# Optimization experiments

Measured on AMD Instinct MI355X. Metric: run time of the kernel, lower is better.

The kernel has to match this reference:

```python
import jax, jax.numpy as jnp
import numpy as np
import math

B, LC, LQ, D = 64, 1024, 128, 128


def setup_inputs() -> dict:
    key = jax.random.key(0)
    k1, k2, k3, k4, k5 = jax.random.split(key, 5)
    c_rep = jax.random.normal(k1, (B, LC, D), dtype=jnp.float32)
    q_rep = jax.random.normal(k2, (B, LQ, D), dtype=jnp.float32)
    c_mask = jax.random.randint(k3, (B, LC), 0, 2, dtype=jnp.int32)
    q_mask = jax.random.randint(k4, (B, LQ), 0, 2, dtype=jnp.int32)
    lim = math.sqrt(1.0 / D)
    w = jax.random.uniform(k5, (3 * D,), dtype=jnp.float32, minval=-lim, maxval=lim)
    return {"c_rep": c_rep, "q_rep": q_rep, "c_mask": c_mask, "q_mask": q_mask, "w": w}


def _mask_logits(t, m):
    # mask == 1 means masked (matches original: target*(1-mask) + mask*-1e30)
    return t * (1.0 - m) + m * (-1e30)


def reference(c_rep, q_rep, c_mask, q_mask, w):
    d = c_rep.shape[-1]
    w1, w2, w3 = w[:d], w[d:2 * d], w[2 * d:]
    # Trilinear similarity S[b,i,j] = <ct,w1> + <qt,w2> + <ct*qt,w3>
    # computed without materializing the [B,Lc,Lq,3D] concat tensor.
    S = (c_rep @ w1)[:, :, None] \
        + (q_rep @ w2)[:, None, :] \
        + jnp.einsum('bid,bjd->bij', c_rep * w3, q_rep)  # [B, Lc, Lq]
    qm = q_mask[:, None, :].astype(S.dtype)  # [B, 1, Lq]
    cm = c_mask[:, :, None].astype(S.dtype)  # [B, Lc, 1]
    S1 = jax.nn.softmax(_mask_logits(S, qm), axis=2)  # softmax over query dim
    S2 = jax.nn.softmax(_mask_logits(S, cm), axis=1)  # softmax over context dim
    A = jnp.einsum('bij,bjd->bid', S1, q_rep)  # [B, Lc, D]
    # B_att = S1 @ S2^T @ c_rep, associated right-first to avoid [B,Lc,Lc]
    T = jnp.einsum('bkj,bkd->bjd', S2, c_rep)  # [B, Lq, D]
    B_att = jnp.einsum('bij,bjd->bid', S1, T)  # [B, Lc, D]
    out = jnp.concatenate([c_rep, A, c_rep * A, c_rep * B_att], axis=2)  # [B, Lc, 4D]
    # dropout is identity at inference
    return out
```

## Files before the change

kernel.cpp:

```cpp
#include <hip/hip_runtime.h>
#include <hip/hip_bf16.h>
#include <cstdint>
#include <cstddef>

#define B_   64
#define LC_  1024
#define LQ_  128
#define D_   128

typedef __bf16 bf16;
typedef bf16  bf16x8 __attribute__((ext_vector_type(8)));
typedef bf16  bf16x4 __attribute__((ext_vector_type(4)));
typedef float f32x4  __attribute__((ext_vector_type(4)));

__device__ __forceinline__ f32x4 mfma16(bf16x8 a, bf16x8 b, f32x4 c) {
  return __builtin_amdgcn_mfma_f32_16x16x32_bf16(a, b, c, 0, 0, 0);
}

__device__ __forceinline__ int swz(int row, int elem) { return elem ^ ((row & 7) << 3); }

__global__ __launch_bounds__(256) void kpre(const float* __restrict__ c, const float* __restrict__ q,
                                            const float* __restrict__ w,
                                            float* __restrict__ cw1, bf16* __restrict__ cw3,
                                            bf16* __restrict__ cT,
                                            float* __restrict__ qw2, bf16* __restrict__ qb,
                                            bf16* __restrict__ qT) {
  __shared__ float wA[128];
  __shared__ float wB[128];
  __shared__ bf16  tile[128 * 136];
  const int b = blockIdx.y, bx = blockIdx.x;
  const int t = threadIdx.x;

  if (bx < 8) {
    const int k0 = bx * 128;
    if (t < 128) { wA[t] = w[t]; wB[t] = w[256 + t]; }
    __syncthreads();
    {
      const int r = t >> 1, d0 = (t & 1) * 64;
      const float* crow = c + ((size_t)(b * LC_ + k0 + r) * D_ + d0);
      bf16* orow = cw3 + ((size_t)(b * LC_ + k0 + r) * D_ + d0);
      float dot = 0.f;
#pragma unroll
      for (int v = 0; v < 8; ++v) {
        const float4 f0 = ((const float4*)crow)[v * 2 + 0];
        const float4 f1 = ((const float4*)crow)[v * 2 + 1];
        const int dd = d0 + v * 8;
        dot += f0.x * wA[dd + 0] + f0.y * wA[dd + 1] + f0.z * wA[dd + 2] + f0.w * wA[dd + 3]
             + f1.x * wA[dd + 4] + f1.y * wA[dd + 5] + f1.z * wA[dd + 6] + f1.w * wA[dd + 7];
        bf16x8 oc, o;
        oc[0] = (bf16)f0.x; oc[1] = (bf16)f0.y; oc[2] = (bf16)f0.z; oc[3] = (bf16)f0.w;
        oc[4] = (bf16)f1.x; oc[5] = (bf16)f1.y; oc[6] = (bf16)f1.z; oc[7] = (bf16)f1.w;
        o[0] = (bf16)(f0.x * wB[dd + 0]); o[1] = (bf16)(f0.y * wB[dd + 1]);
        o[2] = (bf16)(f0.z * wB[dd + 2]); o[3] = (bf16)(f0.w * wB[dd + 3]);
        o[4] = (bf16)(f1.x * wB[dd + 4]); o[5] = (bf16)(f1.y * wB[dd + 5]);
        o[6] = (bf16)(f1.z * wB[dd + 6]); o[7] = (bf16)(f1.w * wB[dd + 7]);
        *(bf16x8*)&tile[r * 136 + dd] = oc;
        *(bf16x8*)(orow + v * 8) = o;
      }
      dot += __shfl_xor(dot, 1);
      if ((t & 1) == 0) cw1[b * LC_ + k0 + r] = dot;
    }
    __syncthreads();
    {
      const int d = t >> 1, kh = (t & 1) * 64;
      bf16* trow = cT + ((size_t)(b * D_ + d) * LC_ + k0 + kh);
#pragma unroll
      for (int v = 0; v < 8; ++v) {
        bf16x8 o;
#pragma unroll
        for (int e = 0; e < 8; ++e) o[e] = tile[(kh + v * 8 + e) * 136 + d];
        *(bf16x8*)(trow + v * 8) = o;
      }
    }
  } else {
    if (t < 128) wA[t] = w[128 + t];
    __syncthreads();
    {
      const int r = t >> 1, d0 = (t & 1) * 64;
      const float* qrow = q + ((size_t)(b * LQ_ + r) * D_ + d0);
      bf16* orow = qb + ((size_t)(b * LQ_ + r) * D_ + d0);
      float dot = 0.f;
#pragma unroll
      for (int v = 0; v < 8; ++v) {
        const float4 f0 = ((const float4*)qrow)[v * 2 + 0];
        const float4 f1 = ((const float4*)qrow)[v * 2 + 1];
        const int dd = d0 + v * 8;
        dot += f0.x * wA[dd + 0] + f0.y * wA[dd + 1] + f0.z * wA[dd + 2] + f0.w * wA[dd + 3]
             + f1.x * wA[dd + 4] + f1.y * wA[dd + 5] + f1.z * wA[dd + 6] + f1.w * wA[dd + 7];
        bf16x8 o;
        o[0] = (bf16)f0.x; o[1] = (bf16)f0.y; o[2] = (bf16)f0.z; o[3] = (bf16)f0.w;
        o[4] = (bf16)f1.x; o[5] = (bf16)f1.y; o[6] = (bf16)f1.z; o[7] = (bf16)f1.w;
        *(bf16x8*)&tile[r * 136 + dd] = o;
        *(bf16x8*)(orow + v * 8) = o;
      }
      dot += __shfl_xor(dot, 1);
      if ((t & 1) == 0) qw2[b * LQ_ + r] = dot;
    }
    __syncthreads();
    {
      const int d = t >> 1, jh = (t & 1) * 64;
      bf16* trow = qT + ((size_t)(b * D_ + d) * LQ_ + jh);
#pragma unroll
      for (int v = 0; v < 8; ++v) {
        bf16x8 o;
#pragma unroll
        for (int e = 0; e < 8; ++e) o[e] = tile[(jh + v * 8 + e) * 136 + d];
        *(bf16x8*)(trow + v * 8) = o;
      }
    }
  }
}

__global__ __launch_bounds__(256) void k1(const float* __restrict__ cw1, const float* __restrict__ qw2,
                                          const int* __restrict__ cmask,
                                          const bf16* __restrict__ cw3, const bf16* __restrict__ cT,
                                          const bf16* __restrict__ qb,
                                          float* __restrict__ Tpart, float* __restrict__ lpart) {
  __shared__ bf16  qs[64 * 128];
  __shared__ bf16  PT[64 * 64];
  __shared__ float lred[4][64];
  const int bx = blockIdx.x;
  const int ks = bx >> 1, jh = bx & 1;
  const int b = blockIdx.y;
  const int j0g = jh * 64;
  const int t = threadIdx.x;
  const int wk = t >> 6, lane = t & 63, quad = lane >> 4, l15 = lane & 15;

#pragma unroll
  for (int idx = t; idx < 1024; idx += 256) {
    const int row = idx >> 4, ch = idx & 15;
    *(bf16x8*)&qs[row * 128 + swz(row, ch * 8)] =
        *(const bf16x8*)(qb + ((size_t)(b * LQ_ + j0g + row) * D_ + ch * 8));
  }
  const f32x4 z = {0.f, 0.f, 0.f, 0.f};
  f32x4 Tacc[4][2];
#pragma unroll
  for (int jt = 0; jt < 4; ++jt) { Tacc[jt][0] = z; Tacc[jt][1] = z; }
  float lacc[4] = {0.f, 0.f, 0.f, 0.f};
  float qv[4];
#pragma unroll
  for (int jt = 0; jt < 4; ++jt) qv[jt] = qw2[b * LQ_ + j0g + jt * 16 + l15];
  __syncthreads();

  for (int kt = 0; kt < 2; ++kt) {
    const int k0g = ks * 128 + kt * 64;

    f32x4 S[4] = {z, z, z, z};
#pragma unroll
    for (int kk = 0; kk < 4; ++kk) {
      const bf16x8 a = *(const bf16x8*)(cw3 +
          ((size_t)(b * LC_ + k0g + wk * 16 + l15) * D_ + kk * 32 + quad * 8));
#pragma unroll
      for (int jt = 0; jt < 4; ++jt) {
        const int jr = jt * 16 + l15;
        const bf16x8 bq = *(const bf16x8*)&qs[jr * 128 + swz(jr, kk * 32 + quad * 8)];
        S[jt] = mfma16(a, bq, S[jt]);
      }
    }
    float c1v[4]; int cmv[4];
#pragma unroll
    for (int rr = 0; rr < 4; ++rr) {
      const int krow = k0g + wk * 16 + quad * 4 + rr;
      c1v[rr] = cw1[b * LC_ + krow];
      cmv[rr] = cmask[b * LC_ + krow];
    }
#pragma unroll
    for (int jt = 0; jt < 4; ++jt) {
      bf16x4 pk;
#pragma unroll
      for (int rr = 0; rr < 4; ++rr) {
        const float p = cmv[rr] ? 0.f : __expf(S[jt][rr] + c1v[rr] + qv[jt]);
        lacc[jt] += p;
        pk[rr] = (bf16)p;
      }
      const int jr = jt * 16 + l15;
      *(bf16x4*)&PT[jr * 64 + swz(jr, wk * 16 + quad * 4)] = pk;
    }
    __syncthreads();

#pragma unroll
    for (int kk = 0; kk < 2; ++kk) {
      const bf16x8 bd0 = *(const bf16x8*)(cT +
          ((size_t)(b * D_ + wk * 32 + l15) * LC_ + k0g + kk * 32 + quad * 8));
      const bf16x8 bd1 = *(const bf16x8*)(cT +
          ((size_t)(b * D_ + wk * 32 + 16 + l15) * LC_ + k0g + kk * 32 + quad * 8));
#pragma unroll
      for (int jt = 0; jt < 4; ++jt) {
        const int jr = jt * 16 + l15;
        const bf16x8 aP = *(const bf16x8*)&PT[jr * 64 + swz(jr, kk * 32 + quad * 8)];
        Tacc[jt][0] = mfma16(aP, bd0, Tacc[jt][0]);
        Tacc[jt][1] = mfma16(aP, bd1, Tacc[jt][1]);
      }
    }
    __syncthreads();
  }

#pragma unroll
  for (int jt = 0; jt < 4; ++jt) {
    lacc[jt] += __shfl_xor(lacc[jt], 16);
    lacc[jt] += __shfl_xor(lacc[jt], 32);
  }
  if (lane < 16) {
#pragma unroll
    for (int jt = 0; jt < 4; ++jt) lred[wk][jt * 16 + l15] = lacc[jt];
  }
  __syncthreads();
  if (t < 64)
    lpart[(size_t)(b * 8 + ks) * 128 + j0g + t] =
        lred[0][t] + lred[1][t] + lred[2][t] + lred[3][t];

  float* tp = Tpart + ((size_t)(b * 8 + ks)) * (128 * 128);
#pragma unroll
  for (int jt = 0; jt < 4; ++jt)
#pragma unroll
    for (int dt = 0; dt < 2; ++dt)
#pragma unroll
      for (int rr = 0; rr < 4; ++rr)
        tp[(j0g + jt * 16 + quad * 4 + rr) * 128 + wk * 32 + dt * 16 + l15] =
            Tacc[jt][dt][rr];
}

__global__ __launch_bounds__(512) void k1r(const float* __restrict__ Tpart,
                                           const float* __restrict__ lpart,
                                           bf16* __restrict__ TT) {
  __shared__ float Tsum[32 * 132];
  __shared__ float linv[32];
  const int js = blockIdx.x, b = blockIdx.y;
  const int j0 = js * 32;
  const int t = threadIdx.x;
#pragma unroll
  for (int idx = t; idx < 1024; idx += 512) {
    const int row = idx >> 5, seg = idx & 31;
    float4 s = {0.f, 0.f, 0.f, 0.f};
#pragma unroll
    for (int i = 0; i < 8; ++i) {
      const float4 v = ((const float4*)(Tpart + ((size_t)(b * 8 + i)) * (128 * 128)) + j0 * 32)[idx];
      s.x += v.x; s.y += v.y; s.z += v.z; s.w += v.w;
    }
    *(float4*)&Tsum[row * 132 + seg * 4] = s;
  }
  if (t < 32) {
    float l = 0.f;
#pragma unroll
    for (int i = 0; i < 8; ++i) l += lpart[(size_t)(b * 8 + i) * 128 + j0 + t];
    linv[t] = 1.f / l;
  }
  __syncthreads();
  if (t < 256) {
    const int d = t >> 1, jhh = (t & 1) * 16;
    bf16x8 o0, o1;
#pragma unroll
    for (int e = 0; e < 8; ++e) {
      o0[e] = (bf16)(Tsum[(jhh + e) * 132 + d] * linv[jhh + e]);
      o1[e] = (bf16)(Tsum[(jhh + 8 + e) * 132 + d] * linv[jhh + 8 + e]);
    }
    bf16* dst = TT + ((size_t)(b * D_ + d) * LQ_ + j0 + jhh);
    *(bf16x8*)dst = o0;
    *(bf16x8*)(dst + 8) = o1;
  }
}

__global__ __launch_bounds__(256, 4) void k2(const float* __restrict__ c, const float* __restrict__ cw1,
                                             const float* __restrict__ qw2, const int* __restrict__ qmask,
                                             const bf16* __restrict__ cw3, const bf16* __restrict__ qb,
                                             const bf16* __restrict__ qT, const bf16* __restrict__ TT,
                                             float* __restrict__ out) {
  __shared__ __align__(16) char smem[37888];
  bf16* qTs = (bf16*)(smem);
  bf16* TTs = (bf16*)(smem + 16384);
  bf16* P1  = (bf16*)(smem + 32768);
  float* A32 = (float*)(smem);
  float* B32 = (float*)(smem + 16896);
  const int it = blockIdx.x, b = blockIdx.y;
  const int i0 = it * 64;
  const int t = threadIdx.x;
  const int w = t >> 6, lane = t & 63, quad = lane >> 4, l15 = lane & 15;

  bf16x8 aF[4];
#pragma unroll
  for (int kk = 0; kk < 4; ++kk)
    aF[kk] = *(const bf16x8*)(cw3 +
        ((size_t)(b * LC_ + i0 + w * 16 + l15) * D_ + kk * 32 + quad * 8));
  float c1v[4];
#pragma unroll
  for (int rr = 0; rr < 4; ++rr)
    c1v[rr] = cw1[b * LC_ + i0 + w * 16 + quad * 4 + rr];

  const f32x4 z = {0.f, 0.f, 0.f, 0.f};
  f32x4 Aacc[8], Bacc[8];
#pragma unroll
  for (int n = 0; n < 8; ++n) { Aacc[n] = z; Bacc[n] = z; }
  float lacc[4] = {0.f, 0.f, 0.f, 0.f};

#pragma unroll
  for (int jh = 0; jh < 2; ++jh) {
#pragma unroll
    for (int idx = t; idx < 1024; idx += 256) {
      const int row = idx >> 3, ch = idx & 7;
      const int sc = (ch * 8) ^ ((row & 7) << 3);
      *(bf16x8*)&qTs[row * 64 + sc] =
          *(const bf16x8*)(qT + ((size_t)(b * D_ + row) * LQ_ + jh * 64 + ch * 8));
      *(bf16x8*)&TTs[row * 64 + sc] =
          *(const bf16x8*)(TT + ((size_t)(b * D_ + row) * LQ_ + jh * 64 + ch * 8));
    }
    __syncthreads();

#pragma unroll
    for (int jtl = 0; jtl < 2; ++jtl) {
      const int j0 = jh * 64 + jtl * 32;
      const float qv0 = qw2[b * LQ_ + j0 + l15];
      const float qv1 = qw2[b * LQ_ + j0 + 16 + l15];
      const int   qm0 = qmask[b * LQ_ + j0 + l15];
      const int   qm1 = qmask[b * LQ_ + j0 + 16 + l15];

      f32x4 S0 = z, S1 = z;
#pragma unroll
      for (int kk = 0; kk < 4; ++kk) {
        const bf16x8 b0 = *(const bf16x8*)(qb +
            ((size_t)(b * LQ_ + j0 + l15) * D_ + kk * 32 + quad * 8));
        const bf16x8 b1 = *(const bf16x8*)(qb +
            ((size_t)(b * LQ_ + j0 + 16 + l15) * D_ + kk * 32 + quad * 8));
        S0 = mfma16(aF[kk], b0, S0);
        S1 = mfma16(aF[kk], b1, S1);
      }
#pragma unroll
      for (int rr = 0; rr < 4; ++rr) {
        const float p0 = qm0 ? 0.f : __expf(S0[rr] + c1v[rr] + qv0);
        const float p1 = qm1 ? 0.f : __expf(S1[rr] + c1v[rr] + qv1);
        lacc[rr] += p0 + p1;
        P1[(w * 16 + quad * 4 + rr) * 40 + l15] = (bf16)p0;
        P1[(w * 16 + quad * 4 + rr) * 40 + 16 + l15] = (bf16)p1;
      }
      __syncthreads();

      const bf16x8 aP = *(bf16x8*)&P1[(w * 16 + l15) * 40 + quad * 8];
      const int cbase = jtl * 32 + quad * 8;
#pragma unroll
      for (int nt = 0; nt < 8; ++nt) {
        const int row = nt * 16 + l15;
        const int sc = cbase ^ ((row & 7) << 3);
        const bf16x8 bq = *(bf16x8*)&qTs[row * 64 + sc];
        const bf16x8 bt = *(bf16x8*)&TTs[row * 64 + sc];
        Aacc[nt] = mfma16(aP, bq, Aacc[nt]);
        Bacc[nt] = mfma16(aP, bt, Bacc[nt]);
      }
      __syncthreads();
    }
  }

#pragma unroll
  for (int rr = 0; rr < 4; ++rr) {
    float v = lacc[rr];
    v += __shfl_xor(v, 1); v += __shfl_xor(v, 2);
    v += __shfl_xor(v, 4); v += __shfl_xor(v, 8);
    lacc[rr] = 1.f / v;
  }

#pragma unroll
  for (int h = 0; h < 2; ++h) {
    if ((w >> 1) == h) {
      const int lrow0 = (w & 1) * 16 + quad * 4;
#pragma unroll
      for (int nt = 0; nt < 8; ++nt)
#pragma unroll
        for (int rr = 0; rr < 4; ++rr) {
          A32[(lrow0 + rr) * 132 + nt * 16 + l15] = Aacc[nt][rr] * lacc[rr];
          B32[(lrow0 + rr) * 132 + nt * 16 + l15] = Bacc[nt][rr] * lacc[rr];
        }
    }
    __syncthreads();
#pragma unroll
    for (int idx = t; idx < 1024; idx += 256) {
      const int lrow = idx >> 5, seg = idx & 31;
      const size_t grow = (size_t)(b * LC_ + i0 + h * 32 + lrow);
      const float4 c4 = ((const float4*)(c + grow * D_))[seg];
      const float4 a4 = *(float4*)&A32[lrow * 132 + seg * 4];
      const float4 b4 = *(float4*)&B32[lrow * 132 + seg * 4];
      float4* ob = (float4*)(out + grow * 512);
      ob[seg] = c4;
      ob[32 + seg] = a4;
      float4 ca; ca.x = c4.x * a4.x; ca.y = c4.y * a4.y; ca.z = c4.z * a4.z; ca.w = c4.w * a4.w;
      ob[64 + seg] = ca;
      float4 cb; cb.x = c4.x * b4.x; cb.y = c4.y * b4.y; cb.z = c4.z * b4.z; cb.w = c4.w * b4.w;
      ob[96 + seg] = cb;
    }
    __syncthreads();
  }
}

extern "C" void kernel_launch(void* const* d_in, const int* in_sizes, int n_in,
                              void* d_out, int out_size, void* d_ws, size_t ws_size,
                              hipStream_t stream) {
  (void)in_sizes; (void)n_in; (void)out_size; (void)ws_size;
  const float* c     = (const float*)d_in[0];
  const float* q     = (const float*)d_in[1];
  const int*   cmask = (const int*)d_in[2];
  const int*   qmask = (const int*)d_in[3];
  const float* w     = (const float*)d_in[4];
  float* out = (float*)d_out;

  char* ws = (char*)d_ws;
  float* cw1 = (float*)(ws + 0);
  float* qw2 = (float*)(ws + 262144);
  bf16*  cw3 = (bf16*)(ws + 294912);
  bf16*  cT  = (bf16*)(ws + 17072128);
  bf16*  qb  = (bf16*)(ws + 33849344);
  bf16*  qT  = (bf16*)(ws + 35946496);
  bf16*  TT  = (bf16*)(ws + 38043648);

  float* Tpart = out;
  float* lpart = out + 8388608;

  kpre<<<dim3(9, 64), 256, 0, stream>>>(c, q, w, cw1, cw3, cT, qw2, qb, qT);
  k1  <<<dim3(16, 64), 256, 0, stream>>>(cw1, qw2, cmask, cw3, cT, qb, Tpart, lpart);
  k1r <<<dim3(4, 64), 512, 0, stream>>>(Tpart, lpart, TT);
  k2  <<<dim3(16, 64), 256, 0, stream>>>(c, cw1, qw2, qmask, cw3, qb, qT, TT, out);
}
```

Measured before the change: 237.7 us.

## Drop transposed context copy; feed T-GEMM directly from fp32 context via K16 MFMA

The preprocessing kernel no longer writes a bf16 transposed copy of the context. k1 now builds the T = S2^T·C product straight from register-held P fragments and strided fp32 context loads, converted on the fly for a 16x16x16 MFMA. This removes the shared-memory P round-trip and its barriers. k1's grid is re-split into 32 query-row slices per batch, with the per-warp T partials reduced through shared-memory atomics. Separately, k2 drops two barriers per inner step. The price is uncoalesced strided global loads of c, shared atomics and more blocks, and the k2 barrier removal risks a race on the P1 buffer.

```diff
diff --git a/kernel.cpp b/kernel.cpp
--- a/kernel.cpp
+++ b/kernel.cpp
@@ -12,9 +12,22 @@
 typedef bf16  bf16x8 __attribute__((ext_vector_type(8)));
 typedef bf16  bf16x4 __attribute__((ext_vector_type(4)));
 typedef float f32x4  __attribute__((ext_vector_type(4)));
+typedef short s16x4  __attribute__((ext_vector_type(4)));
 
 __device__ __forceinline__ f32x4 mfma16(bf16x8 a, bf16x8 b, f32x4 c) {
   return __builtin_amdgcn_mfma_f32_16x16x32_bf16(a, b, c, 0, 0, 0);
+}
+__device__ __forceinline__ f32x4 mfma16k16(s16x4 a, s16x4 b, f32x4 c) {
+#if __has_builtin(__builtin_amdgcn_mfma_f32_16x16x16bf16_1k)
+  return __builtin_amdgcn_mfma_f32_16x16x16bf16_1k(a, b, c, 0, 0, 0);
+#else
+  asm("v_mfma_f32_16x16x16_bf16 %0, %1, %2, %0" : "+v"(c) : "v"(a), "v"(b));
+  return c;
+#endif
+}
+__device__ __forceinline__ short bfbits(float x) {
+  bf16 h = (bf16)x;
+  return __builtin_bit_cast(short, h);
 }
 
 __device__ __forceinline__ int swz(int row, int elem) { return elem ^ ((row & 7) << 3); }
@@ -22,7 +35,6 @@
 __global__ __launch_bounds__(256) void kpre(const float* __restrict__ c, const float* __restrict__ q,
                                             const float* __restrict__ w,
                                             float* __restrict__ cw1, bf16* __restrict__ cw3,
-                                            bf16* __restrict__ cT,
                                             float* __restrict__ qw2, bf16* __restrict__ qb,
                                             bf16* __restrict__ qT) {
   __shared__ float wA[128];
@@ -35,43 +47,26 @@
     const int k0 = bx * 128;
     if (t < 128) { wA[t] = w[t]; wB[t] = w[256 + t]; }
     __syncthreads();
-    {
-      const int r = t >> 1, d0 = (t & 1) * 64;
-      const float* crow = c + ((size_t)(b * LC_ + k0 + r) * D_ + d0);
-      bf16* orow = cw3 + ((size_t)(b * LC_ + k0 + r) * D_ + d0);
-      float dot = 0.f;
-#pragma unroll
-      for (int v = 0; v < 8; ++v) {
-        const float4 f0 = ((const float4*)crow)[v * 2 + 0];
-        const float4 f1 = ((const float4*)crow)[v * 2 + 1];
-        const int dd = d0 + v * 8;
-        dot += f0.x * wA[dd + 0] + f0.y * wA[dd + 1] + f0.z * wA[dd + 2] + f0.w * wA[dd + 3]
-             + f1.x * wA[dd + 4] + f1.y * wA[dd + 5] + f1.z * wA[dd + 6] + f1.w * wA[dd + 7];
-        bf16x8 oc, o;
-        oc[0] = (bf16)f0.x; oc[1] = (bf16)f0.y; oc[2] = (bf16)f0.z; oc[3] = (bf16)f0.w;
-        oc[4] = (bf16)f1.x; oc[5] = (bf16)f1.y; oc[6] = (bf16)f1.z; oc[7] = (bf16)f1.w;
-        o[0] = (bf16)(f0.x * wB[dd + 0]); o[1] = (bf16)(f0.y * wB[dd + 1]);
-        o[2] = (bf16)(f0.z * wB[dd + 2]); o[3] = (bf16)(f0.w * wB[dd + 3]);
-        o[4] = (bf16)(f1.x * wB[dd + 4]); o[5] = (bf16)(f1.y * wB[dd + 5]);
-        o[6] = (bf16)(f1.z * wB[dd + 6]); o[7] = (bf16)(f1.w * wB[dd + 7]);
-        *(bf16x8*)&tile[r * 136 + dd] = oc;
-        *(bf16x8*)(orow + v * 8) = o;
-      }
-      dot += __shfl_xor(dot, 1);
-      if ((t & 1) == 0) cw1[b * LC_ + k0 + r] = dot;
-    }
-    __syncthreads();
-    {
-      const int d = t >> 1, kh = (t & 1) * 64;
-      bf16* trow = cT + ((size_t)(b * D_ + d) * LC_ + k0 + kh);
-#pragma unroll
-      for (int v = 0; v < 8; ++v) {
-        bf16x8 o;
-#pragma unroll
-        for (int e = 0; e < 8; ++e) o[e] = tile[(kh + v * 8 + e) * 136 + d];
-        *(bf16x8*)(trow + v * 8) = o;
-      }
-    }
+    const int r = t >> 1, d0 = (t & 1) * 64;
+    const float* crow = c + ((size_t)(b * LC_ + k0 + r) * D_ + d0);
+    bf16* orow = cw3 + ((size_t)(b * LC_ + k0 + r) * D_ + d0);
+    float dot = 0.f;
+#pragma unroll
+    for (int v = 0; v < 8; ++v) {
+      const float4 f0 = ((const float4*)crow)[v * 2 + 0];
+      const float4 f1 = ((const float4*)crow)[v * 2 + 1];
+      const int dd = d0 + v * 8;
+      dot += f0.x * wA[dd + 0] + f0.y * wA[dd + 1] + f0.z * wA[dd + 2] + f0.w * wA[dd + 3]
+           + f1.x * wA[dd + 4] + f1.y * wA[dd + 5] + f1.z * wA[dd + 6] + f1.w * wA[dd + 7];
+      bf16x8 o;
+      o[0] = (bf16)(f0.x * wB[dd + 0]); o[1] = (bf16)(f0.y * wB[dd + 1]);
+      o[2] = (bf16)(f0.z * wB[dd + 2]); o[3] = (bf16)(f0.w * wB[dd + 3]);
+      o[4] = (bf16)(f1.x * wB[dd + 4]); o[5] = (bf16)(f1.y * wB[dd + 5]);
+      o[6] = (bf16)(f1.z * wB[dd + 6]); o[7] = (bf16)(f1.w * wB[dd + 7]);
+      *(bf16x8*)(orow + v * 8) = o;
+    }
+    dot += __shfl_xor(dot, 1);
+    if ((t & 1) == 0) cw1[b * LC_ + k0 + r] = dot;
   } else {
     if (t < 128) wA[t] = w[128 + t];
     __syncthreads();
@@ -111,47 +106,50 @@
   }
 }
 
-__global__ __launch_bounds__(256) void k1(const float* __restrict__ cw1, const float* __restrict__ qw2,
-                                          const int* __restrict__ cmask,
-                                          const bf16* __restrict__ cw3, const bf16* __restrict__ cT,
-                                          const bf16* __restrict__ qb,
-                                          float* __restrict__ Tpart, float* __restrict__ lpart) {
-  __shared__ bf16  qs[64 * 128];
-  __shared__ bf16  PT[64 * 64];
-  __shared__ float lred[4][64];
+__global__ __launch_bounds__(256, 4) void k1(const float* __restrict__ cw1, const float* __restrict__ qw2,
+                                             const int* __restrict__ cmask,
+                                             const bf16* __restrict__ cw3, const float* __restrict__ c,
+                                             const bf16* __restrict__ qb,
+                                             float* __restrict__ Tpart, float* __restrict__ lpart) {
+  __shared__ __align__(16) char smem[16384 + 512];
+  bf16*  qs   = (bf16*)smem;
+  float* Tsum = (float*)smem;
+  float* lred = (float*)(smem + 16384);
   const int bx = blockIdx.x;
-  const int ks = bx >> 1, jh = bx & 1;
+  const int ks = bx >> 2, js = bx & 3;
   const int b = blockIdx.y;
-  const int j0g = jh * 64;
+  const int j0 = js * 32;
   const int t = threadIdx.x;
   const int wk = t >> 6, lane = t & 63, quad = lane >> 4, l15 = lane & 15;
 
 #pragma unroll
-  for (int idx = t; idx < 1024; idx += 256) {
+  for (int idx = t; idx < 512; idx += 256) {
     const int row = idx >> 4, ch = idx & 15;
     *(bf16x8*)&qs[row * 128 + swz(row, ch * 8)] =
-        *(const bf16x8*)(qb + ((size_t)(b * LQ_ + j0g + row) * D_ + ch * 8));
+        *(const bf16x8*)(qb + ((size_t)(b * LQ_ + j0 + row) * D_ + ch * 8));
   }
   const f32x4 z = {0.f, 0.f, 0.f, 0.f};
-  f32x4 Tacc[4][2];
-#pragma unroll
-  for (int jt = 0; jt < 4; ++jt) { Tacc[jt][0] = z; Tacc[jt][1] = z; }
-  float lacc[4] = {0.f, 0.f, 0.f, 0.f};
-  float qv[4];
-#pragma unroll
-  for (int jt = 0; jt < 4; ++jt) qv[jt] = qw2[b * LQ_ + j0g + jt * 16 + l15];
+  f32x4 Tacc[2][8];
+#pragma unroll
+  for (int jt = 0; jt < 2; ++jt)
+#pragma unroll
+    for (int dt = 0; dt < 8; ++dt) Tacc[jt][dt] = z;
+  float lacc[2] = {0.f, 0.f};
+  float qv[2];
+#pragma unroll
+  for (int jt = 0; jt < 2; ++jt) qv[jt] = qw2[b * LQ_ + j0 + jt * 16 + l15];
   __syncthreads();
 
   for (int kt = 0; kt < 2; ++kt) {
-    const int k0g = ks * 128 + kt * 64;
-
-    f32x4 S[4] = {z, z, z, z};
+    const int krow_base = ks * 128 + kt * 64 + wk * 16;
+
+    f32x4 S[2] = {z, z};
 #pragma unroll
     for (int kk = 0; kk < 4; ++kk) {
       const bf16x8 a = *(const bf16x8*)(cw3 +
-          ((size_t)(b * LC_ + k0g + wk * 16 + l15) * D_ + kk * 32 + quad * 8));
-#pragma unroll
-      for (int jt = 0; jt < 4; ++jt) {
+          ((size_t)(b * LC_ + krow_base + l15) * D_ + kk * 32 + quad * 8));
+#pragma unroll
+      for (int jt = 0; jt < 2; ++jt) {
         const int jr = jt * 16 + l15;
         const bf16x8 bq = *(const bf16x8*)&qs[jr * 128 + swz(jr, kk * 32 + quad * 8)];
         S[jt] = mfma16(a, bq, S[jt]);
@@ -160,64 +158,59 @@
     float c1v[4]; int cmv[4];
 #pragma unroll
     for (int rr = 0; rr < 4; ++rr) {
-      const int krow = k0g + wk * 16 + quad * 4 + rr;
+      const int krow = krow_base + quad * 4 + rr;
       c1v[rr] = cw1[b * LC_ + krow];
       cmv[rr] = cmask[b * LC_ + krow];
     }
-#pragma unroll
-    for (int jt = 0; jt < 4; ++jt) {
-      bf16x4 pk;
+    s16x4 pk[2];
+#pragma unroll
+    for (int jt = 0; jt < 2; ++jt)
 #pragma unroll
       for (int rr = 0; rr < 4; ++rr) {
         const float p = cmv[rr] ? 0.f : __expf(S[jt][rr] + c1v[rr] + qv[jt]);
         lacc[jt] += p;
-        pk[rr] = (bf16)p;
-      }
-      const int jr = jt * 16 + l15;
-      *(bf16x4*)&PT[jr * 64 + swz(jr, wk * 16 + quad * 4)] = pk;
-    }
-    __syncthreads();
-
-#pragma unroll
-    for (int kk = 0; kk < 2; ++kk) {
-      const bf16x8 bd0 = *(const bf16x8*)(cT +
-          ((size_t)(b * D_ + wk * 32 + l15) * LC_ + k0g + kk * 32 + quad * 8));
-      const bf16x8 bd1 = *(const bf16x8*)(cT +
-          ((size_t)(b * D_ + wk * 32 + 16 + l15) * LC_ + k0g + kk * 32 + quad * 8));
-#pragma unroll
-      for (int jt = 0; jt < 4; ++jt) {
-        const int jr = jt * 16 + l15;
-        const bf16x8 aP = *(const bf16x8*)&PT[jr * 64 + swz(jr, kk * 32 + quad * 8)];
-        Tacc[jt][0] = mfma16(aP, bd0, Tacc[jt][0]);
-        Tacc[jt][1] = mfma16(aP, bd1, Tacc[jt][1]);
-      }
-    }
-    __syncthreads();
-  }
-
-#pragma unroll
-  for (int jt = 0; jt < 4; ++jt) {
+        pk[jt][rr] = bfbits(p);
+      }
+    const float* crow0 = c + ((size_t)(b * LC_ + krow_base + quad * 4) * D_ + l15);
+#pragma unroll
+    for (int dt = 0; dt < 8; ++dt) {
+      s16x4 bd;
+#pragma unroll
+      for (int e = 0; e < 4; ++e) bd[e] = bfbits(crow0[e * D_ + dt * 16]);
+      Tacc[0][dt] = mfma16k16(pk[0], bd, Tacc[0][dt]);
+      Tacc[1][dt] = mfma16k16(pk[1], bd, Tacc[1][dt]);
+    }
+  }
+
+#pragma unroll
+  for (int jt = 0; jt < 2; ++jt) {
     lacc[jt] += __shfl_xor(lacc[jt], 16);
     lacc[jt] += __shfl_xor(lacc[jt], 32);
   }
   if (lane < 16) {
 #pragma unroll
-    for (int jt = 0; jt < 4; ++jt) lred[wk][jt * 16 + l15] = lacc[jt];
-  }
-  __syncthreads();
-  if (t < 64)
-    lpart[(size_t)(b * 8 + ks) * 128 + j0g + t] =
-        lred[0][t] + lred[1][t] + lred[2][t] + lred[3][t];
-
-  float* tp = Tpart + ((size_t)(b * 8 + ks)) * (128 * 128);
-#pragma unroll
-  for (int jt = 0; jt < 4; ++jt)
-#pragma unroll
-    for (int dt = 0; dt < 2; ++dt)
+    for (int jt = 0; jt < 2; ++jt) lred[wk * 32 + jt * 16 + l15] = lacc[jt];
+  }
+  __syncthreads();
+  if (t < 32)
+    lpart[(size_t)(b * 8 + ks) * 128 + j0 + t] =
+        lred[0 * 32 + t] + lred[1 * 32 + t] + lred[2 * 32 + t] + lred[3 * 32 + t];
+
+#pragma unroll
+  for (int idx = t; idx < 1024; idx += 256) ((f32x4*)Tsum)[idx] = z;
+  __syncthreads();
+#pragma unroll
+  for (int jt = 0; jt < 2; ++jt)
+#pragma unroll
+    for (int dt = 0; dt < 8; ++dt)
 #pragma unroll
       for (int rr = 0; rr < 4; ++rr)
-        tp[(j0g + jt * 16 + quad * 4 + rr) * 128 + wk * 32 + dt * 16 + l15] =
-            Tacc[jt][dt][rr];
+        atomicAdd(&Tsum[(jt * 16 + quad * 4 + rr) * 128 + dt * 16 + l15], Tacc[jt][dt][rr]);
+  __syncthreads();
+  float* tp = Tpart + ((size_t)(b * 8 + ks)) * (128 * 128) + (size_t)j0 * 128;
+#pragma unroll
+  for (int idx = t; idx < 1024; idx += 256)
+    ((float4*)tp)[idx] = ((const float4*)Tsum)[idx];
 }
 
 __global__ __launch_bounds__(512) void k1r(const float* __restrict__ Tpart,
@@ -294,6 +287,7 @@
 
 #pragma unroll
   for (int jh = 0; jh < 2; ++jh) {
+    if (jh) __syncthreads();
 #pragma unroll
     for (int idx = t; idx < 1024; idx += 256) {
       const int row = idx >> 3, ch = idx & 7;
@@ -331,8 +325,6 @@
         P1[(w * 16 + quad * 4 + rr) * 40 + l15] = (bf16)p0;
         P1[(w * 16 + quad * 4 + rr) * 40 + 16 + l15] = (bf16)p1;
       }
-      __syncthreads();
-
       const bf16x8 aP = *(bf16x8*)&P1[(w * 16 + l15) * 40 + quad * 8];
       const int cbase = jtl * 32 + quad * 8;
 #pragma unroll
@@ -344,7 +336,6 @@
         Aacc[nt] = mfma16(aP, bq, Aacc[nt]);
         Bacc[nt] = mfma16(aP, bt, Bacc[nt]);
       }
-      __syncthreads();
     }
   }
 
@@ -356,6 +347,7 @@
     lacc[rr] = 1.f / v;
   }
 
+  __syncthreads();
 #pragma unroll
   for (int h = 0; h < 2; ++h) {
     if ((w >> 1) == h) {
@@ -403,16 +395,15 @@
   float* cw1 = (float*)(ws + 0);
   float* qw2 = (float*)(ws + 262144);
   bf16*  cw3 = (bf16*)(ws + 294912);
-  bf16*  cT  = (bf16*)(ws + 17072128);
-  bf16*  qb  = (bf16*)(ws + 33849344);
-  bf16*  qT  = (bf16*)(ws + 35946496);
-  bf16*  TT  = (bf16*)(ws + 38043648);
+  bf16*  qb  = (bf16*)(ws + 17072128);
+  bf16*  qT  = (bf16*)(ws + 19169280);
+  bf16*  TT  = (bf16*)(ws + 21266432);
 
   float* Tpart = out;
   float* lpart = out + 8388608;
 
-  kpre<<<dim3(9, 64), 256, 0, stream>>>(c, q, w, cw1, cw3, cT, qw2, qb, qT);
-  k1  <<<dim3(16, 64), 256, 0, stream>>>(cw1, qw2, cmask, cw3, cT, qb, Tpart, lpart);
+  kpre<<<dim3(9, 64), 256, 0, stream>>>(c, q, w, cw1, cw3, qw2, qb, qT);
+  k1  <<<dim3(32, 64), 256, 0, stream>>>(cw1, qw2, cmask, cw3, c, qb, Tpart, lpart);
   k1r <<<dim3(4, 64), 512, 0, stream>>>(Tpart, lpart, TT);
   k2  <<<dim3(16, 64), 256, 0, stream>>>(c, cw1, qw2, qmask, cw3, qb, qT, TT, out);
 }
```

Result: slower. 400.6 us (+68.5%).
